# Performance work log

Hardware: AMD Instinct MI355X
Metric: run time of the kernel (lower is better)

Reference implementation:

```python
import jax, jax.numpy as jnp
import numpy as np

BETA = 0.001  # l2 regularization coefficient from __init__
N_SEG = 4096


def _pair_indices(cu):
    # Build global pair index arrays (pos<neg within each segment),
    # equivalent to torch.combinations(arange(L), 2) per segment.
    cache = {}
    pos_l, neg_l, seg_l = [], [], []
    for s in range(len(cu) - 1):
        a, b = int(cu[s]), int(cu[s + 1])
        L = b - a
        if L not in cache:
            cache[L] = np.triu_indices(L, 1)
        i, j = cache[L]
        pos_l.append(a + i)
        neg_l.append(a + j)
        seg_l.append(np.full(i.shape[0], s, dtype=np.int64))
    pos = np.concatenate(pos_l).astype(np.int64)
    neg = np.concatenate(neg_l).astype(np.int64)
    seg = np.concatenate(seg_l)
    counts = np.bincount(seg, minlength=len(cu) - 1).astype(np.float32)
    return pos, neg, seg, counts


def setup_inputs() -> dict:
    key = jax.random.key(0)
    rng = np.random.default_rng(0)
    lengths = rng.integers(32, 128, N_SEG)  # variable candidates per prompt
    cu = np.concatenate([[0], np.cumsum(lengths)]).astype(np.int64)
    n = int(cu[-1])
    logits = jax.random.normal(key, (n,), dtype=jnp.float32)
    return {"logits": logits, "cu_lengths": jnp.asarray(cu)}


def reference(logits, cu_lengths):
    cu = np.asarray(jax.device_get(cu_lengths))  # boundaries are static ints
    pos_idx, neg_idx, seg_id, counts = _pair_indices(cu)
    pos_idx = jnp.asarray(pos_idx)
    neg_idx = jnp.asarray(neg_idx)
    seg_id = jnp.asarray(seg_id)
    counts = jnp.asarray(counts)

    pos = logits[pos_idx]  # [P]
    neg = logits[neg_idx]  # [P]
    l2 = 0.5 * (pos * pos + neg * neg)
    pair_loss = -jax.nn.log_sigmoid(pos - neg) + BETA * l2  # [P]
    # per-segment mean, then mean over segments (reduction='mean')
    seg_sum = jax.ops.segment_sum(pair_loss, seg_id, num_segments=len(cu) - 1)
    per_seg = seg_sum / counts
    return jnp.mean(per_seg)
```

## Files before the change

### kernel.cpp

```cpp
#include <hip/hip_runtime.h>
#include <math.h>

#define BETA 0.001f
#define WPB  4

__global__ __launch_bounds__(WPB * 64) void rmloss_seg_kernel(
    const float* __restrict__ logits,
    const int*   __restrict__ cu,
    float*       __restrict__ partial,
    int n_seg)
{
    const int wave = threadIdx.x >> 6;
    const int lane = threadIdx.x & 63;
    const int s = blockIdx.x * WPB + wave;
    if (s >= n_seg) return;

    const int a   = cu[s];
    const int L   = cu[s + 1] - a;
    const int Lm1 = L - 1;

    __shared__ float xs[WPB][128];
    float* __restrict__ x = xs[wave];

    const bool a_ok = lane < L;
    const bool b_ok = lane + 64 < L;
    const float va = a_ok ? logits[a + lane] : 0.0f;
    const float vb = b_ok ? logits[a + lane + 64] : 0.0f;
    x[lane]      = va;
    x[lane + 64] = vb;
    __builtin_amdgcn_wave_barrier();

    const float kNL2E = -1.44269504088896340736f;
    const float kT2L2 =  1.38629436111989061883f;

    float acc_a = 0.0f, acc_b = 0.0f;
    if (L > 64) {
        #pragma unroll 4
        for (int j = 0; j < L; ++j) {
            const float v = x[j];
            float ua = fabsf(va - v);
            float ea = __builtin_amdgcn_exp2f(ua * kNL2E);
            acc_a += ua;
            acc_a = fmaf(kT2L2, __builtin_amdgcn_logf(1.0f + ea), acc_a);
            float ub = fabsf(vb - v);
            float eb = __builtin_amdgcn_exp2f(ub * kNL2E);
            acc_b += ub;
            acc_b = fmaf(kT2L2, __builtin_amdgcn_logf(1.0f + eb), acc_b);
        }
    } else {
        #pragma unroll 4
        for (int j = 0; j < L; ++j) {
            const float v = x[j];
            float ua = fabsf(va - v);
            float ea = __builtin_amdgcn_exp2f(ua * kNL2E);
            acc_a += ua;
            acc_a = fmaf(kT2L2, __builtin_amdgcn_logf(1.0f + ea), acc_a);
        }
    }

    const float acch = (a_ok ? acc_a : 0.0f) + (b_ok ? acc_b : 0.0f);
    const float lin  = va * (float)(2 * lane - Lm1)
                     + vb * (float)(2 * (lane + 64) - Lm1);
    const float sq   = va * va + vb * vb;

    float f = 0.25f * acch + 0.5f * lin + (0.5f * BETA * (float)Lm1) * sq;
    #pragma unroll
    for (int off = 32; off > 0; off >>= 1)
        f += __shfl_down(f, off, 64);

    if (lane == 0) {
        const float P = 0.5f * (float)(L * Lm1);
        const float diag = 0.25f * (float)L * kT2L2;
        partial[s] = (f - diag) / P;
    }
}

__global__ __launch_bounds__(1024) void rmloss_reduce_kernel(
    const float* __restrict__ partial, float* __restrict__ out,
    int n, float inv_n)
{
    float acc = 0.0f;
    for (int k = threadIdx.x; k < n; k += 1024) acc += partial[k];
    #pragma unroll
    for (int off = 32; off > 0; off >>= 1) acc += __shfl_down(acc, off, 64);

    __shared__ float r[16];
    const int lane = threadIdx.x & 63;
    const int wid  = threadIdx.x >> 6;
    if (lane == 0) r[wid] = acc;
    __syncthreads();
    if (threadIdx.x == 0) {
        float t = 0.0f;
        #pragma unroll
        for (int w = 0; w < 16; ++w) t += r[w];
        out[0] = t * inv_n;
    }
}

extern "C" void kernel_launch(void* const* d_in, const int* in_sizes, int n_in,
                              void* d_out, int out_size, void* d_ws, size_t ws_size,
                              hipStream_t stream) {
    (void)n_in; (void)out_size; (void)ws_size;

    const float* logits  = (const float*)d_in[0];
    const int*   cu      = (const int*)d_in[1];
    float*       out     = (float*)d_out;
    float*       partial = (float*)d_ws;

    const int n_seg  = in_sizes[1] - 1;
    const int blocks = (n_seg + WPB - 1) / WPB;

    rmloss_seg_kernel<<<blocks, WPB * 64, 0, stream>>>(logits, cu, partial, n_seg);
    rmloss_reduce_kernel<<<1, 1024, 0, stream>>>(partial, out, n_seg,
                                                 1.0f / (float)n_seg);
}
```

Measured before the change: 73.50 us.

## Replace per-pair log with running product and fuse final reduction via atomics

Accumulates the product of (1+exp(-|d|)) terms and takes one log per lane instead of a log per pair, halving transcendental work in the inner loop. It also removes the separate reduction kernel, having each block atomically add its scaled partial sum to the output after a memset. The product could overflow or lose precision for long segments with small differences, and float atomics make the summation order nondeterministic.

Result: no change. 72.34 us (-1.6%).

```diff
diff --git a/kernel.cpp b/kernel.cpp
--- a/kernel.cpp
+++ b/kernel.cpp
@@ -4,113 +4,106 @@
 #define BETA 0.001f
 #define WPB  4
 
-__global__ __launch_bounds__(WPB * 64) void rmloss_seg_kernel(
+__global__ __launch_bounds__(WPB * 64) void rmloss_kernel(
     const float* __restrict__ logits,
     const int*   __restrict__ cu,
-    float*       __restrict__ partial,
-    int n_seg)
+    float*       __restrict__ out,
+    int n_seg, float inv_n)
 {
     const int wave = threadIdx.x >> 6;
     const int lane = threadIdx.x & 63;
     const int s = blockIdx.x * WPB + wave;
-    if (s >= n_seg) return;
-
-    const int a   = cu[s];
-    const int L   = cu[s + 1] - a;
-    const int Lm1 = L - 1;
 
     __shared__ float xs[WPB][128];
-    float* __restrict__ x = xs[wave];
-
-    const bool a_ok = lane < L;
-    const bool b_ok = lane + 64 < L;
-    const float va = a_ok ? logits[a + lane] : 0.0f;
-    const float vb = b_ok ? logits[a + lane + 64] : 0.0f;
-    x[lane]      = va;
-    x[lane + 64] = vb;
-    __builtin_amdgcn_wave_barrier();
+    __shared__ float wsum[WPB];
 
     const float kNL2E = -1.44269504088896340736f;
     const float kT2L2 =  1.38629436111989061883f;
 
-    float acc_a = 0.0f, acc_b = 0.0f;
-    if (L > 64) {
-        #pragma unroll 4
-        for (int j = 0; j < L; ++j) {
-            const float v = x[j];
-            float ua = fabsf(va - v);
-            float ea = __builtin_amdgcn_exp2f(ua * kNL2E);
-            acc_a += ua;
-            acc_a = fmaf(kT2L2, __builtin_amdgcn_logf(1.0f + ea), acc_a);
-            float ub = fabsf(vb - v);
-            float eb = __builtin_amdgcn_exp2f(ub * kNL2E);
-            acc_b += ub;
-            acc_b = fmaf(kT2L2, __builtin_amdgcn_logf(1.0f + eb), acc_b);
+    float segval = 0.0f;
+
+    if (s < n_seg) {
+        const int a   = cu[s];
+        const int L   = cu[s + 1] - a;
+        const int Lm1 = L - 1;
+
+        float* __restrict__ x = xs[wave];
+
+        const bool a_ok = lane < L;
+        const bool b_ok = lane + 64 < L;
+        const float va = a_ok ? logits[a + lane] : 0.0f;
+        const float vb = b_ok ? logits[a + lane + 64] : 0.0f;
+        x[lane]      = va;
+        x[lane + 64] = vb;
+        __builtin_amdgcn_wave_barrier();
+
+        float su_a = 0.0f, p_a = 1.0f;
+        float su_b = 0.0f, p_b = 1.0f;
+
+        if (L > 64) {
+            #pragma unroll 4
+            for (int j = 0; j < L; ++j) {
+                const float v = x[j];
+                const float ua = fabsf(va - v);
+                const float ea = __builtin_amdgcn_exp2f(ua * kNL2E);
+                su_a += ua;
+                p_a  *= 1.0f + ea;
+                const float ub = fabsf(vb - v);
+                const float eb = __builtin_amdgcn_exp2f(ub * kNL2E);
+                su_b += ub;
+                p_b  *= 1.0f + eb;
+            }
+        } else {
+            #pragma unroll 4
+            for (int j = 0; j < L; ++j) {
+                const float v = x[j];
+                const float ua = fabsf(va - v);
+                const float ea = __builtin_amdgcn_exp2f(ua * kNL2E);
+                su_a += ua;
+                p_a  *= 1.0f + ea;
+            }
         }
-    } else {
-        #pragma unroll 4
-        for (int j = 0; j < L; ++j) {
-            const float v = x[j];
-            float ua = fabsf(va - v);
-            float ea = __builtin_amdgcn_exp2f(ua * kNL2E);
-            acc_a += ua;
-            acc_a = fmaf(kT2L2, __builtin_amdgcn_logf(1.0f + ea), acc_a);
+
+        const float ha = su_a + kT2L2 * __builtin_amdgcn_logf(p_a);
+        const float hb = su_b + kT2L2 * __builtin_amdgcn_logf(p_b);
+        const float acch = (a_ok ? ha : 0.0f) + (b_ok ? hb : 0.0f);
+
+        const float lin = va * (float)(2 * lane - Lm1)
+                        + vb * (float)(2 * (lane + 64) - Lm1);
+        const float sq  = va * va + vb * vb;
+
+        float f = 0.25f * acch + 0.5f * lin + (0.5f * BETA * (float)Lm1) * sq;
+        #pragma unroll
+        for (int off = 32; off > 0; off >>= 1)
+            f += __shfl_down(f, off, 64);
+
+        if (lane == 0) {
+            const float P    = 0.5f * (float)(L * Lm1);
+            const float diag = 0.25f * (float)L * kT2L2;
+            segval = (f - diag) / P * inv_n;
         }
     }
 
-    const float acch = (a_ok ? acc_a : 0.0f) + (b_ok ? acc_b : 0.0f);
-    const float lin  = va * (float)(2 * lane - Lm1)
-                     + vb * (float)(2 * (lane + 64) - Lm1);
-    const float sq   = va * va + vb * vb;
-
-    float f = 0.25f * acch + 0.5f * lin + (0.5f * BETA * (float)Lm1) * sq;
-    #pragma unroll
-    for (int off = 32; off > 0; off >>= 1)
-        f += __shfl_down(f, off, 64);
-
-    if (lane == 0) {
-        const float P = 0.5f * (float)(L * Lm1);
-        const float diag = 0.25f * (float)L * kT2L2;
-        partial[s] = (f - diag) / P;
-    }
-}
-
-__global__ __launch_bounds__(1024) void rmloss_reduce_kernel(
-    const float* __restrict__ partial, float* __restrict__ out,
-    int n, float inv_n)
-{
-    float acc = 0.0f;
-    for (int k = threadIdx.x; k < n; k += 1024) acc += partial[k];
-    #pragma unroll
-    for (int off = 32; off > 0; off >>= 1) acc += __shfl_down(acc, off, 64);
-
-    __shared__ float r[16];
-    const int lane = threadIdx.x & 63;
-    const int wid  = threadIdx.x >> 6;
-    if (lane == 0) r[wid] = acc;
+    if (lane == 0) wsum[wave] = segval;
     __syncthreads();
     if (threadIdx.x == 0) {
-        float t = 0.0f;
-        #pragma unroll
-        for (int w = 0; w < 16; ++w) t += r[w];
-        out[0] = t * inv_n;
+        atomicAdd(out, wsum[0] + wsum[1] + wsum[2] + wsum[3]);
     }
 }
 
 extern "C" void kernel_launch(void* const* d_in, const int* in_sizes, int n_in,
                               void* d_out, int out_size, void* d_ws, size_t ws_size,
                               hipStream_t stream) {
-    (void)n_in; (void)out_size; (void)ws_size;
+    (void)n_in; (void)out_size; (void)d_ws; (void)ws_size;
 
-    const float* logits  = (const float*)d_in[0];
-    const int*   cu      = (const int*)d_in[1];
-    float*       out     = (float*)d_out;
-    float*       partial = (float*)d_ws;
+    const float* logits = (const float*)d_in[0];
+    const int*   cu     = (const int*)d_in[1];
+    float*       out    = (float*)d_out;
 
     const int n_seg  = in_sizes[1] - 1;
     const int blocks = (n_seg + WPB - 1) / WPB;
 
-    rmloss_seg_kernel<<<blocks, WPB * 64, 0, stream>>>(logits, cu, partial, n_seg);
-    rmloss_reduce_kernel<<<1, 1024, 0, stream>>>(partial, out, n_seg,
-                                                 1.0f / (float)n_seg);
+    hipMemsetAsync(out, 0, sizeof(float), stream);
+    rmloss_kernel<<<blocks, WPB * 64, 0, stream>>>(logits, cu, out, n_seg,
+                                                   1.0f / (float)n_seg);
 }
```
